# Optimization experiments

Hardware: AMD Instinct MI355X
Metric: run time of the kernel (lower is better)

Reference implementation:

```python
import jax, jax.numpy as jnp
import numpy as np

E = 1_000_000   # edges (temporal neighbor facts)
D = 128         # emb_dim
N = 200_000     # nodes carrying hidden state
B = 512         # queries (batch)
R = 240         # num_rel -> rel table has 2R+1 rows
T = 100_000     # tail nodes (scatter output size)


def setup_inputs() -> dict:
    key = jax.random.key(0)
    ks = jax.random.split(key, 14)
    b_col  = jax.random.randint(ks[0], (E,), 0, B)
    n_col  = jax.random.randint(ks[1], (E,), 0, N)
    h_col  = jax.random.randint(ks[2], (E,), 0, N)
    r_col  = jax.random.randint(ks[3], (E,), 0, 2 * R)   # r+1 in [1, 2R]
    t_col  = jax.random.randint(ks[4], (E,), 0, N)
    ts_col = jax.random.randint(ks[5], (E,), 0, 1000)
    facts = jnp.stack([b_col, n_col, h_col, r_col, t_col, ts_col], axis=1)
    s = 1.0 / np.sqrt(D)
    return {
        "hidden":     jax.random.normal(ks[6], (N, D), jnp.float32) * 0.02,
        "rel_table":  jax.random.normal(ks[7], (2 * R + 1, D), jnp.float32) * 0.02,
        "Ws":         jax.random.normal(ks[8], (D, D), jnp.float32) * s,
        "Wr":         jax.random.normal(ks[9], (D, D), jnp.float32) * s,
        "Wqr_w":      jax.random.normal(ks[10], (D, D), jnp.float32) * s,
        "Wqr_b":      jnp.zeros((D,), jnp.float32),
        "wa_w":       jax.random.normal(ks[11], (D, 1), jnp.float32) * s,
        "wa_b":       jnp.zeros((1,), jnp.float32),
        "Wh":         jax.random.normal(ks[12], (D, D), jnp.float32) * s,
        "query_rel":  jax.random.randint(ks[13], (B,), 0, 2 * R),
        "facts":      facts,
        "tail_index": jax.random.randint(jax.random.fold_in(key, 99), (E,), 0, T),
        "tail_nodes": jnp.arange(T),
    }


def reference(hidden, rel_table, Ws, Wr, Wqr_w, Wqr_b, wa_w, wa_b, Wh,
              query_rel, facts, tail_index, tail_nodes):
    b = facts[:, 0]
    n = facts[:, 1]
    r = facts[:, 3]
    h_e = hidden[n]                      # [E, D] gather node hidden
    hr  = rel_table[r + 1]               # [E, D] gather relation emb
    q_r = rel_table[query_rel + 1][b]    # [E, D] per-edge query relation
    # attention MLP: sigmoid(w_alpha(relu(Ws h + Wr r + Wqr q + b)))
    pre = h_e @ Ws + hr @ Wr + (q_r @ Wqr_w + Wqr_b)          # [E, D]
    alpha = jax.nn.sigmoid(jax.nn.relu(pre) @ wa_w + wa_b)    # [E, 1]
    message = alpha * (h_e + hr)                              # [E, D]
    agg = jax.ops.segment_sum(message, tail_index,
                              num_segments=tail_nodes.shape[0])  # [T, D]
    return agg @ Wh                      # act = identity (default)
```

## Files before the change

### kernel.cpp

```cpp
#include <hip/hip_runtime.h>
#include <hip/hip_fp16.h>
#include <math.h>

#define DD 128
#define CAP 64

typedef _Float16 half_t;
typedef __attribute__((ext_vector_type(8))) _Float16 half8;
typedef __attribute__((ext_vector_type(4))) float floatx4;

#define LDW 136

__device__ __forceinline__ __half2 relu2(__half2 x) {
    return __hmul2(x, __hgt2(x, __float2half2_rn(0.f)));
}

template <int CTRL>
__device__ __forceinline__ float dpp_add(float x) {
    int y = __builtin_amdgcn_update_dpp(0, __float_as_int(x), CTRL, 0xf, 0xf, true);
    return x + __int_as_float(y);
}

__global__ void wt4(const float* __restrict__ W0, const float* __restrict__ W1,
                    const float* __restrict__ W2, const float* __restrict__ W3,
                    half_t* __restrict__ T0, half_t* __restrict__ T1,
                    half_t* __restrict__ T2, half_t* __restrict__ T3) {
    const float* W = blockIdx.x == 0 ? W0 : blockIdx.x == 1 ? W1 : blockIdx.x == 2 ? W2 : W3;
    half_t* T      = blockIdx.x == 0 ? T0 : blockIdx.x == 1 ? T1 : blockIdx.x == 2 ? T2 : T3;
    for (int i = threadIdx.x; i < DD * DD; i += blockDim.x) {
        int n = i >> 7, k = i & 127;
        T[i] = (half_t)W[(size_t)k * DD + n];
    }
}

__device__ __forceinline__ void mfma_pass_store(
    const half_t* As, const half_t* WT, int tileM, int M, int w, int lane,
    __half* Packed, int halfOff) {
    int rowf = lane & 15;
    int kgrp = (lane >> 4) * 8;
    floatx4 acc[8];
#pragma unroll
    for (int t = 0; t < 8; t++) acc[t] = (floatx4){0.f, 0.f, 0.f, 0.f};
    const half_t* ap = As + (w * 16 + rowf) * LDW + kgrp;
    const half_t* bp0 = WT + rowf * LDW + kgrp;
#pragma unroll
    for (int kk = 0; kk < DD; kk += 32) {
        half8 a = *(const half8*)(ap + kk);
#pragma unroll
        for (int t = 0; t < 8; t++) {
            half8 b = *(const half8*)(bp0 + t * 16 * LDW + kk);
            acc[t] = __builtin_amdgcn_mfma_f32_16x16x32_f16(a, b, acc[t], 0, 0, 0);
        }
    }
    int orow = tileM + w * 16 + (lane >> 4) * 4;
#pragma unroll
    for (int t = 0; t < 8; t++) {
        int col = t * 16 + rowf;
#pragma unroll
        for (int i = 0; i < 4; i++) {
            int gr = orow + i;
            if (gr < M) Packed[(size_t)gr * 256 + halfOff + col] = __float2half(acc[t][i]);
        }
    }
}

__global__ __launch_bounds__(256) void gemm_pack2(
    const float* __restrict__ table, int M,
    const half_t* __restrict__ WT1_g, const half_t* __restrict__ WT2_g,
    __half* __restrict__ Packed) {
    __shared__ half_t WT[DD * LDW];
    __shared__ half_t As[64 * LDW];
    int tid = threadIdx.x;
    int lane = tid & 63;
    int w = tid >> 6;
    int tileM = blockIdx.x * 64;

    for (int i = tid; i < 2048; i += 256) {
        int row = i >> 5, c4 = i & 31;
        int gr = tileM + row;
        float4 v = make_float4(0.f, 0.f, 0.f, 0.f);
        if (gr < M) v = *(const float4*)(table + (size_t)gr * DD + c4 * 4);
        __half2 h01 = __floats2half2_rn(v.x, v.y);
        __half2 h23 = __floats2half2_rn(v.z, v.w);
        *(uint2*)(As + row * LDW + c4 * 4) = make_uint2(*(unsigned*)&h01, *(unsigned*)&h23);
    }
    for (int i = tid; i < 2048; i += 256) {
        int n = i >> 4, ch = i & 15;
        *(half8*)(WT + n * LDW + ch * 8) = *(const half8*)(WT1_g + n * DD + ch * 8);
    }
    __syncthreads();
    mfma_pass_store(As, WT, tileM, M, w, lane, Packed, 0);
    __syncthreads();
    for (int i = tid; i < 2048; i += 256) {
        int n = i >> 4, ch = i & 15;
        *(half8*)(WT + n * LDW + ch * 8) = *(const half8*)(WT2_g + n * DD + ch * 8);
    }
    __syncthreads();
    mfma_pass_store(As, WT, tileM, M, w, lane, Packed, 128);
}

__global__ __launch_bounds__(256) void gemm_mfma(
    const float* __restrict__ table, const int* __restrict__ idx, int idxAdd, int M,
    const half_t* __restrict__ WT_g, const float* __restrict__ bias,
    float* __restrict__ OutF, __half* __restrict__ OutH) {
    __shared__ half_t WT[DD * LDW];
    __shared__ half_t As[64 * LDW];
    int tid = threadIdx.x;
    int lane = tid & 63;
    int w = tid >> 6;
    int rowf = lane & 15;
    int kgrp = (lane >> 4) * 8;

    for (int i = tid; i < 2048; i += 256) {
        int n = i >> 4, ch = i & 15;
        *(half8*)(WT + n * LDW + ch * 8) = *(const half8*)(WT_g + n * DD + ch * 8);
    }
    int tileM = blockIdx.x * 64;
    for (int i = tid; i < 2048; i += 256) {
        int row = i >> 5, c4 = i & 31;
        int gr = tileM + row;
        float4 v = make_float4(0.f, 0.f, 0.f, 0.f);
        if (gr < M) {
            int src = idx ? (idx[gr] + idxAdd) : gr;
            v = *(const float4*)(table + (size_t)src * DD + c4 * 4);
        }
        __half2 h01 = __floats2half2_rn(v.x, v.y);
        __half2 h23 = __floats2half2_rn(v.z, v.w);
        *(uint2*)(As + row * LDW + c4 * 4) = make_uint2(*(unsigned*)&h01, *(unsigned*)&h23);
    }
    __syncthreads();

    floatx4 acc[8];
#pragma unroll
    for (int t = 0; t < 8; t++) acc[t] = (floatx4){0.f, 0.f, 0.f, 0.f};
    const half_t* ap = As + (w * 16 + rowf) * LDW + kgrp;
    const half_t* bp0 = WT + rowf * LDW + kgrp;
#pragma unroll
    for (int kk = 0; kk < DD; kk += 32) {
        half8 a = *(const half8*)(ap + kk);
#pragma unroll
        for (int t = 0; t < 8; t++) {
            half8 b = *(const half8*)(bp0 + t * 16 * LDW + kk);
            acc[t] = __builtin_amdgcn_mfma_f32_16x16x32_f16(a, b, acc[t], 0, 0, 0);
        }
    }
    int orow = tileM + w * 16 + (lane >> 4) * 4;
#pragma unroll
    for (int t = 0; t < 8; t++) {
        int col = t * 16 + rowf;
        float bv = bias ? bias[col] : 0.f;
#pragma unroll
        for (int i = 0; i < 4; i++) {
            int gr = orow + i;
            if (gr < M) {
                float o = acc[t][i] + bv;
                if (OutF) OutF[(size_t)gr * DD + col] = o;
                if (OutH) OutH[(size_t)gr * DD + col] = __float2half(o);
            }
        }
    }
}

__global__ __launch_bounds__(256) void alpha_scatter(
    const __half* __restrict__ HB, const __half* __restrict__ RB,
    const __half* __restrict__ QB, const int* __restrict__ facts,
    const int* __restrict__ tail, const float* __restrict__ wa,
    const float* __restrict__ wa_b,
    int* __restrict__ cursor, int2* __restrict__ meta, int E) {
    int tid = threadIdx.x;
    int lane = tid & 63;
    int g = lane >> 4;
    int cl = lane & 15;
    int c = cl * 8;
    int wv = (blockIdx.x * 256 + tid) >> 6;
    int e0 = wv * 8 + g;

    float4 wva = *(const float4*)(wa + c);
    float4 wvb = *(const float4*)(wa + c + 4);
    __half2 w0 = __halves2half2(__float2half(wva.x), __float2half(wva.y));
    __half2 w1 = __halves2half2(__float2half(wva.z), __float2half(wva.w));
    __half2 w2 = __halves2half2(__float2half(wvb.x), __float2half(wvb.y));
    __half2 w3 = __halves2half2(__float2half(wvb.z), __float2half(wvb.w));
    float wb = wa_b[0];

    int f0 = e0, f1 = e0 + 4;
    bool v0 = f0 < E, v1 = f1 < E;
    int fc0 = v0 ? f0 : 0, fc1 = v1 ? f1 : 0;

    int2 bn0 = *(const int2*)(facts + (size_t)fc0 * 6);
    int r0 = facts[(size_t)fc0 * 6 + 3];
    int tl0 = tail[fc0];
    int2 bn1 = *(const int2*)(facts + (size_t)fc1 * 6);
    int r1 = facts[(size_t)fc1 * 6 + 3];
    int tl1 = tail[fc1];

    uint4 h0 = *(const uint4*)(HB + (size_t)bn0.y * 256 + 128 + c);
    uint4 rr0 = *(const uint4*)(RB + (size_t)(r0 + 1) * 256 + 128 + c);
    uint4 q0 = *(const uint4*)(QB + (size_t)bn0.x * DD + c);
    uint4 h1 = *(const uint4*)(HB + (size_t)bn1.y * 256 + 128 + c);
    uint4 rr1 = *(const uint4*)(RB + (size_t)(r1 + 1) * 256 + 128 + c);
    uint4 q1 = *(const uint4*)(QB + (size_t)bn1.x * DD + c);

#define DOT8(hu, ru, qu, out)                                                          \
    {                                                                                  \
        __half2 p0 = relu2(__hadd2(__hadd2(*(__half2*)&(hu).x, *(__half2*)&(ru).x),    \
                                   *(__half2*)&(qu).x));                               \
        __half2 p1 = relu2(__hadd2(__hadd2(*(__half2*)&(hu).y, *(__half2*)&(ru).y),    \
                                   *(__half2*)&(qu).y));                               \
        __half2 p2 = relu2(__hadd2(__hadd2(*(__half2*)&(hu).z, *(__half2*)&(ru).z),    \
                                   *(__half2*)&(qu).z));                               \
        __half2 p3 = relu2(__hadd2(__hadd2(*(__half2*)&(hu).w, *(__half2*)&(ru).w),    \
                                   *(__half2*)&(qu).w));                               \
        __half2 t2 = __hfma2(p1, w1, __hmul2(p0, w0));                                 \
        t2 = __hfma2(p2, w2, t2);                                                      \
        t2 = __hfma2(p3, w3, t2);                                                      \
        out = __half2float(__low2half(t2)) + __half2float(__high2half(t2));            \
    }
    float t0, t1;
    DOT8(h0, rr0, q0, t0);
    DOT8(h1, rr1, q1, t1);
#undef DOT8

    t0 = dpp_add<0x111>(t0); t0 = dpp_add<0x112>(t0);
    t0 = dpp_add<0x114>(t0); t0 = dpp_add<0x118>(t0);
    t1 = dpp_add<0x111>(t1); t1 = dpp_add<0x112>(t1);
    t1 = dpp_add<0x114>(t1); t1 = dpp_add<0x118>(t1);

    if (cl == 15) {
        float a0 = 1.f / (1.f + __expf(-(t0 + wb)));
        float a1 = 1.f / (1.f + __expf(-(t1 + wb)));
        unsigned ab0 = (unsigned)__half_as_ushort(__float2half(a0));
        unsigned ab1 = (unsigned)__half_as_ushort(__float2half(a1));
        if (v0) {
            int slot = atomicAdd(&cursor[tl0], 1);
            if (slot < CAP)
                meta[(size_t)tl0 * CAP + slot] = make_int2(bn0.y, (r0 + 1) | (int)(ab0 << 16));
        }
        if (v1) {
            int slot = atomicAdd(&cursor[tl1], 1);
            if (slot < CAP)
                meta[(size_t)tl1 * CAP + slot] = make_int2(bn1.y, (r1 + 1) | (int)(ab1 << 16));
        }
    }
}

__global__ __launch_bounds__(256) void agg_out(
    const __half* __restrict__ HB, const __half* __restrict__ RB,
    const int2* __restrict__ meta, const int* __restrict__ cursor,
    float* __restrict__ out, int T) {
    int w = threadIdx.x >> 6;
    int lane = threadIdx.x & 63;
    int seg = blockIdx.x * 4 + w;
    if (seg >= T) return;
    int cnt = cursor[seg];
    if (cnt > CAP) cnt = CAP;
    const int2* mp = meta + (size_t)seg * CAP;
    int co = lane * 2;
    float ax = 0.f, ay = 0.f;

#define ACC(hu, ru, y_)                                                        \
    {                                                                          \
        __half2 s = __hadd2(*(__half2*)&(hu), *(__half2*)&(ru));               \
        float al =                                                             \
            __half2float(__ushort_as_half((unsigned short)((unsigned)(y_) >> 16))); \
        float2 sf = __half22float2(s);                                         \
        ax = fmaf(al, sf.x, ax);                                               \
        ay = fmaf(al, sf.y, ay);                                               \
    }

    int i = 0;
    for (; i + 7 < cnt; i += 8) {
        int4 ma = *(const int4*)(mp + i);
        int4 mb = *(const int4*)(mp + i + 2);
        int4 mc = *(const int4*)(mp + i + 4);
        int4 md = *(const int4*)(mp + i + 6);
        unsigned h0 = *(const unsigned*)(HB + (size_t)ma.x * 256 + co);
        unsigned r0 = *(const unsigned*)(RB + (size_t)(ma.y & 0xFFFF) * 256 + co);
        unsigned h1 = *(const unsigned*)(HB + (size_t)ma.z * 256 + co);
        unsigned r1 = *(const unsigned*)(RB + (size_t)(ma.w & 0xFFFF) * 256 + co);
        unsigned h2 = *(const unsigned*)(HB + (size_t)mb.x * 256 + co);
        unsigned r2 = *(const unsigned*)(RB + (size_t)(mb.y & 0xFFFF) * 256 + co);
        unsigned h3 = *(const unsigned*)(HB + (size_t)mb.z * 256 + co);
        unsigned r3 = *(const unsigned*)(RB + (size_t)(mb.w & 0xFFFF) * 256 + co);
        unsigned h4 = *(const unsigned*)(HB + (size_t)mc.x * 256 + co);
        unsigned r4 = *(const unsigned*)(RB + (size_t)(mc.y & 0xFFFF) * 256 + co);
        unsigned h5 = *(const unsigned*)(HB + (size_t)mc.z * 256 + co);
        unsigned r5 = *(const unsigned*)(RB + (size_t)(mc.w & 0xFFFF) * 256 + co);
        unsigned h6 = *(const unsigned*)(HB + (size_t)md.x * 256 + co);
        unsigned r6 = *(const unsigned*)(RB + (size_t)(md.y & 0xFFFF) * 256 + co);
        unsigned h7 = *(const unsigned*)(HB + (size_t)md.z * 256 + co);
        unsigned r7 = *(const unsigned*)(RB + (size_t)(md.w & 0xFFFF) * 256 + co);
        ACC(h0, r0, ma.y); ACC(h1, r1, ma.w);
        ACC(h2, r2, mb.y); ACC(h3, r3, mb.w);
        ACC(h4, r4, mc.y); ACC(h5, r5, mc.w);
        ACC(h6, r6, md.y); ACC(h7, r7, md.w);
    }
    for (; i + 3 < cnt; i += 4) {
        int4 ma = *(const int4*)(mp + i);
        int4 mb = *(const int4*)(mp + i + 2);
        unsigned h0 = *(const unsigned*)(HB + (size_t)ma.x * 256 + co);
        unsigned r0 = *(const unsigned*)(RB + (size_t)(ma.y & 0xFFFF) * 256 + co);
        unsigned h1 = *(const unsigned*)(HB + (size_t)ma.z * 256 + co);
        unsigned r1 = *(const unsigned*)(RB + (size_t)(ma.w & 0xFFFF) * 256 + co);
        unsigned h2 = *(const unsigned*)(HB + (size_t)mb.x * 256 + co);
        unsigned r2 = *(const unsigned*)(RB + (size_t)(mb.y & 0xFFFF) * 256 + co);
        unsigned h3 = *(const unsigned*)(HB + (size_t)mb.z * 256 + co);
        unsigned r3 = *(const unsigned*)(RB + (size_t)(mb.w & 0xFFFF) * 256 + co);
        ACC(h0, r0, ma.y); ACC(h1, r1, ma.w);
        ACC(h2, r2, mb.y); ACC(h3, r3, mb.w);
    }
    for (; i < cnt; i++) {
        int2 m = mp[i];
        unsigned hu = *(const unsigned*)(HB + (size_t)m.x * 256 + co);
        unsigned ru = *(const unsigned*)(RB + (size_t)(m.y & 0xFFFF) * 256 + co);
        ACC(hu, ru, m.y);
    }
#undef ACC

    *(float2*)(out + (size_t)seg * DD + co) = make_float2(ax, ay);
}

extern "C" void kernel_launch(void* const* d_in, const int* in_sizes, int n_in,
                              void* d_out, int out_size, void* d_ws, size_t ws_size,
                              hipStream_t stream) {
    const float* hidden    = (const float*)d_in[0];
    const float* rel_table = (const float*)d_in[1];
    const float* Ws        = (const float*)d_in[2];
    const float* Wr        = (const float*)d_in[3];
    const float* Wqr_w     = (const float*)d_in[4];
    const float* Wqr_b     = (const float*)d_in[5];
    const float* wa_w      = (const float*)d_in[6];
    const float* wa_b      = (const float*)d_in[7];
    const float* Wh        = (const float*)d_in[8];
    const int* query_rel   = (const int*)d_in[9];
    const int* facts       = (const int*)d_in[10];
    const int* tail_index  = (const int*)d_in[11];

    int N     = in_sizes[0] / DD;
    int Rrows = in_sizes[1] / DD;
    int B     = in_sizes[9];
    int E     = in_sizes[11];
    int T     = in_sizes[12];

    char* ws = (char*)d_ws;
    size_t off = 0;
    auto alloc = [&](size_t bytes) -> void* {
        void* p = ws + off;
        off += (bytes + 255) & ~(size_t)255;
        return p;
    };
    __half* HB  = (__half*)alloc((size_t)N * 256 * 2);
    __half* RB  = (__half*)alloc((size_t)Rrows * 256 * 2);
    __half* QB  = (__half*)alloc((size_t)B * DD * 2);
    int* cursor = (int*)alloc((size_t)T * 4);
    int2* meta  = (int2*)alloc((size_t)T * CAP * 8);
    half_t* WsT  = (half_t*)alloc((size_t)DD * DD * 2);
    half_t* WrT  = (half_t*)alloc((size_t)DD * DD * 2);
    half_t* WqrT = (half_t*)alloc((size_t)DD * DD * 2);
    half_t* WhT  = (half_t*)alloc((size_t)DD * DD * 2);

    (void)hipMemsetAsync(cursor, 0, (size_t)T * 4, stream);

    wt4<<<4, 256, 0, stream>>>(Ws, Wr, Wqr_w, Wh, WsT, WrT, WqrT, WhT);

    gemm_pack2<<<(N + 63) / 64, 256, 0, stream>>>(hidden, N, WhT, WsT, HB);
    gemm_pack2<<<(Rrows + 63) / 64, 256, 0, stream>>>(rel_table, Rrows, WhT, WrT, RB);
    gemm_mfma<<<(B + 63) / 64, 256, 0, stream>>>(rel_table, query_rel, 1, B,
                                                 WqrT, Wqr_b, nullptr, QB);

    alpha_scatter<<<(E + 31) / 32, 256, 0, stream>>>(HB, RB, QB, facts, tail_index,
                                                     wa_w, wa_b, cursor, meta, E);

    agg_out<<<(T + 3) / 4, 256, 0, stream>>>(HB, RB, meta, cursor,
                                             (float*)d_out, T);
}
```

Baseline: 451.7 us.

## Stage GEMM outputs through LDS for coalesced stores; process 4 edges per lane group

The packed-GEMM kernel now writes its MFMA accumulators into shared memory first and then stores 16-byte chunks per row to global memory. This replaces scattered 2-byte stores that are strided across rows. Separately, alpha_scatter now handles four edges per 16-lane group instead of two and launches half as many blocks, so more independent gathers are in flight. The cost is extra LDS round trips and barriers in the GEMM, plus higher register pressure in the scatter kernel.

```diff
diff --git a/kernel.cpp b/kernel.cpp
--- a/kernel.cpp
+++ b/kernel.cpp
@@ -33,12 +33,10 @@
     }
 }
 
-__device__ __forceinline__ void mfma_pass_store(
-    const half_t* As, const half_t* WT, int tileM, int M, int w, int lane,
-    __half* Packed, int halfOff) {
+__device__ __forceinline__ void mfma_pass(
+    const half_t* As, const half_t* WT, int w, int lane, floatx4 acc[8]) {
     int rowf = lane & 15;
     int kgrp = (lane >> 4) * 8;
-    floatx4 acc[8];
 #pragma unroll
     for (int t = 0; t < 8; t++) acc[t] = (floatx4){0.f, 0.f, 0.f, 0.f};
     const half_t* ap = As + (w * 16 + rowf) * LDW + kgrp;
@@ -52,14 +50,28 @@
             acc[t] = __builtin_amdgcn_mfma_f32_16x16x32_f16(a, b, acc[t], 0, 0, 0);
         }
     }
-    int orow = tileM + w * 16 + (lane >> 4) * 4;
+}
+
+__device__ __forceinline__ void acc_to_lds(const floatx4 acc[8], half_t* OutT,
+                                           int w, int lane) {
+    int rowf = lane & 15;
+    int rbase = w * 16 + (lane >> 4) * 4;
 #pragma unroll
     for (int t = 0; t < 8; t++) {
         int col = t * 16 + rowf;
 #pragma unroll
-        for (int i = 0; i < 4; i++) {
-            int gr = orow + i;
-            if (gr < M) Packed[(size_t)gr * 256 + halfOff + col] = __float2half(acc[t][i]);
+        for (int i = 0; i < 4; i++) OutT[(rbase + i) * LDW + col] = (half_t)acc[t][i];
+    }
+}
+
+__device__ __forceinline__ void lds_to_packed(const half_t* OutT, int tileM, int M,
+                                              int tid, __half* Packed, int halfOff) {
+    for (int ch = tid; ch < 1024; ch += 256) {
+        int row = ch >> 4, off = (ch & 15) * 8;
+        int gr = tileM + row;
+        if (gr < M) {
+            half8 v = *(const half8*)(OutT + row * LDW + off);
+            *(uint4*)(Packed + (size_t)gr * 256 + halfOff + off) = *(uint4*)&v;
         }
     }
 }
@@ -89,14 +101,23 @@
         *(half8*)(WT + n * LDW + ch * 8) = *(const half8*)(WT1_g + n * DD + ch * 8);
     }
     __syncthreads();
-    mfma_pass_store(As, WT, tileM, M, w, lane, Packed, 0);
+    floatx4 acc[8];
+    mfma_pass(As, WT, w, lane, acc);
+    __syncthreads();
+    acc_to_lds(acc, WT, w, lane);
+    __syncthreads();
+    lds_to_packed(WT, tileM, M, tid, Packed, 0);
     __syncthreads();
     for (int i = tid; i < 2048; i += 256) {
         int n = i >> 4, ch = i & 15;
         *(half8*)(WT + n * LDW + ch * 8) = *(const half8*)(WT2_g + n * DD + ch * 8);
     }
     __syncthreads();
-    mfma_pass_store(As, WT, tileM, M, w, lane, Packed, 128);
+    mfma_pass(As, WT, w, lane, acc);
+    __syncthreads();
+    acc_to_lds(acc, WT, w, lane);
+    __syncthreads();
+    lds_to_packed(WT, tileM, M, tid, Packed, 128);
 }
 
 __global__ __launch_bounds__(256) void gemm_mfma(
@@ -109,7 +130,6 @@
     int lane = tid & 63;
     int w = tid >> 6;
     int rowf = lane & 15;
-    int kgrp = (lane >> 4) * 8;
 
     for (int i = tid; i < 2048; i += 256) {
         int n = i >> 4, ch = i & 15;
@@ -131,19 +151,7 @@
     __syncthreads();
 
     floatx4 acc[8];
-#pragma unroll
-    for (int t = 0; t < 8; t++) acc[t] = (floatx4){0.f, 0.f, 0.f, 0.f};
-    const half_t* ap = As + (w * 16 + rowf) * LDW + kgrp;
-    const half_t* bp0 = WT + rowf * LDW + kgrp;
-#pragma unroll
-    for (int kk = 0; kk < DD; kk += 32) {
-        half8 a = *(const half8*)(ap + kk);
-#pragma unroll
-        for (int t = 0; t < 8; t++) {
-            half8 b = *(const half8*)(bp0 + t * 16 * LDW + kk);
-            acc[t] = __builtin_amdgcn_mfma_f32_16x16x32_f16(a, b, acc[t], 0, 0, 0);
-        }
-    }
+    mfma_pass(As, WT, w, lane, acc);
     int orow = tileM + w * 16 + (lane >> 4) * 4;
 #pragma unroll
     for (int t = 0; t < 8; t++) {
@@ -173,7 +181,7 @@
     int cl = lane & 15;
     int c = cl * 8;
     int wv = (blockIdx.x * 256 + tid) >> 6;
-    int e0 = wv * 8 + g;
+    int e0 = wv * 16 + g;
 
     float4 wva = *(const float4*)(wa + c);
     float4 wvb = *(const float4*)(wa + c + 4);
@@ -183,63 +191,61 @@
     __half2 w3 = __halves2half2(__float2half(wvb.z), __float2half(wvb.w));
     float wb = wa_b[0];
 
-    int f0 = e0, f1 = e0 + 4;
-    bool v0 = f0 < E, v1 = f1 < E;
-    int fc0 = v0 ? f0 : 0, fc1 = v1 ? f1 : 0;
-
-    int2 bn0 = *(const int2*)(facts + (size_t)fc0 * 6);
-    int r0 = facts[(size_t)fc0 * 6 + 3];
-    int tl0 = tail[fc0];
-    int2 bn1 = *(const int2*)(facts + (size_t)fc1 * 6);
-    int r1 = facts[(size_t)fc1 * 6 + 3];
-    int tl1 = tail[fc1];
-
-    uint4 h0 = *(const uint4*)(HB + (size_t)bn0.y * 256 + 128 + c);
-    uint4 rr0 = *(const uint4*)(RB + (size_t)(r0 + 1) * 256 + 128 + c);
-    uint4 q0 = *(const uint4*)(QB + (size_t)bn0.x * DD + c);
-    uint4 h1 = *(const uint4*)(HB + (size_t)bn1.y * 256 + 128 + c);
-    uint4 rr1 = *(const uint4*)(RB + (size_t)(r1 + 1) * 256 + 128 + c);
-    uint4 q1 = *(const uint4*)(QB + (size_t)bn1.x * DD + c);
-
-#define DOT8(hu, ru, qu, out)                                                          \
-    {                                                                                  \
-        __half2 p0 = relu2(__hadd2(__hadd2(*(__half2*)&(hu).x, *(__half2*)&(ru).x),    \
-                                   *(__half2*)&(qu).x));                               \
-        __half2 p1 = relu2(__hadd2(__hadd2(*(__half2*)&(hu).y, *(__half2*)&(ru).y),    \
-                                   *(__half2*)&(qu).y));                               \
-        __half2 p2 = relu2(__hadd2(__hadd2(*(__half2*)&(hu).z, *(__half2*)&(ru).z),    \
-                                   *(__half2*)&(qu).z));                               \
-        __half2 p3 = relu2(__hadd2(__hadd2(*(__half2*)&(hu).w, *(__half2*)&(ru).w),    \
-                                   *(__half2*)&(qu).w));                               \
-        __half2 t2 = __hfma2(p1, w1, __hmul2(p0, w0));                                 \
-        t2 = __hfma2(p2, w2, t2);                                                      \
-        t2 = __hfma2(p3, w3, t2);                                                      \
-        out = __half2float(__low2half(t2)) + __half2float(__high2half(t2));            \
-    }
-    float t0, t1;
-    DOT8(h0, rr0, q0, t0);
-    DOT8(h1, rr1, q1, t1);
-#undef DOT8
-
-    t0 = dpp_add<0x111>(t0); t0 = dpp_add<0x112>(t0);
-    t0 = dpp_add<0x114>(t0); t0 = dpp_add<0x118>(t0);
-    t1 = dpp_add<0x111>(t1); t1 = dpp_add<0x112>(t1);
-    t1 = dpp_add<0x114>(t1); t1 = dpp_add<0x118>(t1);
+    bool v[4]; int2 bn[4]; int r[4]; int tl[4];
+#pragma unroll
+    for (int j = 0; j < 4; j++) {
+        int f = e0 + j * 4;
+        v[j] = f < E;
+        int fc = v[j] ? f : 0;
+        bn[j] = *(const int2*)(facts + (size_t)fc * 6);
+        r[j] = facts[(size_t)fc * 6 + 3];
+        tl[j] = tail[fc];
+    }
+
+    uint4 h[4], rr[4], q[4];
+#pragma unroll
+    for (int j = 0; j < 4; j++) {
+        h[j]  = *(const uint4*)(HB + (size_t)bn[j].y * 256 + 128 + c);
+        rr[j] = *(const uint4*)(RB + (size_t)(r[j] + 1) * 256 + 128 + c);
+        q[j]  = *(const uint4*)(QB + (size_t)bn[j].x * DD + c);
+    }
+
+    float t[4];
+#pragma unroll
+    for (int j = 0; j < 4; j++) {
+        __half2 p0 = relu2(__hadd2(__hadd2(*(__half2*)&h[j].x, *(__half2*)&rr[j].x),
+                                   *(__half2*)&q[j].x));
+        __half2 p1 = relu2(__hadd2(__hadd2(*(__half2*)&h[j].y, *(__half2*)&rr[j].y),
+                                   *(__half2*)&q[j].y));
+        __half2 p2 = relu2(__hadd2(__hadd2(*(__half2*)&h[j].z, *(__half2*)&rr[j].z),
+                                   *(__half2*)&q[j].z));
+        __half2 p3 = relu2(__hadd2(__hadd2(*(__half2*)&h[j].w, *(__half2*)&rr[j].w),
+                                   *(__half2*)&q[j].w));
+        __half2 t2 = __hfma2(p1, w1, __hmul2(p0, w0));
+        t2 = __hfma2(p2, w2, t2);
+        t2 = __hfma2(p3, w3, t2);
+        t[j] = __half2float(__low2half(t2)) + __half2float(__high2half(t2));
+    }
+
+#pragma unroll
+    for (int j = 0; j < 4; j++) {
+        t[j] = dpp_add<0x111>(t[j]);
+        t[j] = dpp_add<0x112>(t[j]);
+        t[j] = dpp_add<0x114>(t[j]);
+        t[j] = dpp_add<0x118>(t[j]);
+    }
 
     if (cl == 15) {
-        float a0 = 1.f / (1.f + __expf(-(t0 + wb)));
-        float a1 = 1.f / (1.f + __expf(-(t1 + wb)));
-        unsigned ab0 = (unsigned)__half_as_ushort(__float2half(a0));
-        unsigned ab1 = (unsigned)__half_as_ushort(__float2half(a1));
-        if (v0) {
-            int slot = atomicAdd(&cursor[tl0], 1);
-            if (slot < CAP)
-                meta[(size_t)tl0 * CAP + slot] = make_int2(bn0.y, (r0 + 1) | (int)(ab0 << 16));
-        }
-        if (v1) {
-            int slot = atomicAdd(&cursor[tl1], 1);
-            if (slot < CAP)
-                meta[(size_t)tl1 * CAP + slot] = make_int2(bn1.y, (r1 + 1) | (int)(ab1 << 16));
+#pragma unroll
+        for (int j = 0; j < 4; j++) {
+            if (v[j]) {
+                float a = 1.f / (1.f + __expf(-(t[j] + wb)));
+                unsigned ab = (unsigned)__half_as_ushort(__float2half(a));
+                int slot = atomicAdd(&cursor[tl[j]], 1);
+                if (slot < CAP)
+                    meta[(size_t)tl[j] * CAP + slot] =
+                        make_int2(bn[j].y, (r[j] + 1) | (int)(ab << 16));
+            }
         }
     }
 }
@@ -368,7 +374,7 @@
     gemm_mfma<<<(B + 63) / 64, 256, 0, stream>>>(rel_table, query_rel, 1, B,
                                                  WqrT, Wqr_b, nullptr, QB);
 
-    alpha_scatter<<<(E + 31) / 32, 256, 0, stream>>>(HB, RB, QB, facts, tail_index,
+    alpha_scatter<<<(E + 63) / 64, 256, 0, stream>>>(HB, RB, QB, facts, tail_index,
                                                      wa_w, wa_b, cursor, meta, E);
 
     agg_out<<<(T + 3) / 4, 256, 0, stream>>>(HB, RB, meta, cursor,
```

Result: no change. 448.2 us (-0.8%).
